# Kernel tuning notes

Measured on AMD Instinct MI355X. Metric: run time of the kernel, lower is better.

Reference implementation:

```python
import jax, jax.numpy as jnp
import numpy as np

T, B, N, D, O = 128, 8, 512, 256, 1


def _xavier(key, shape):
    # matches nn.init.xavier_normal_ (gain=1): std = sqrt(2/(fan_in+fan_out))
    std = np.sqrt(2.0 / (shape[0] + shape[1])).astype(np.float32)
    return jax.random.normal(key, shape, jnp.float32) * std


def setup_inputs() -> dict:
    key = jax.random.key(0)
    ks = jax.random.split(key, 7)
    return {
        "x": jax.random.normal(ks[0], (T, B, D), jnp.float32),
        "w_mult": _xavier(ks[1], (N, D)),
        "b_mult": _xavier(ks[2], (N, 1))[:, 0],   # stored (N,1) in torch; used as bias vector
        "w_add": _xavier(ks[3], (N, N)),
        "b_add": _xavier(ks[4], (N, 1))[:, 0],
        "w_final": _xavier(ks[5], (O, N)),
        "b_final": _xavier(ks[6], (O, 1))[:, 0],
        "lmbda_mult": jnp.float32(1.0),
        "lmbda_add": jnp.float32(1.0),
        "eta_mult": jnp.float32(-0.5),
        "eta_add": jnp.float32(-0.5),
        "Store": 0,
        "Batch": 0,
    }


def reference(x, w_mult, b_mult, w_add, b_add, w_final, b_final,
              lmbda_mult, lmbda_add, eta_mult, eta_add, Store, Batch):
    # Store=False / Batch=False branch of HebbFF, vmapped over B sequences
    # and scanned over T timesteps. Fast-weight state: A_mult [B,N,D], A_add [B,N,N].
    Bt = x.shape[1]
    Nh, Dd = w_mult.shape
    lam_m = jax.nn.sigmoid(lmbda_mult)
    lam_a = jax.nn.sigmoid(lmbda_add)

    def step(carry, x_t):
        A_m, A_a = carry                      # [B,N,D], [B,N,N]
        # h_mult = tanh((w_mult * A_mult) @ x + w_mult @ x + b_mult)
        h_m = jnp.tanh(jnp.einsum('bnd,bd->bn', w_mult * A_m, x_t)
                       + x_t @ w_mult.T + b_mult)          # [B,N]
        A_m = lam_m * A_m + eta_mult * jnp.einsum('bn,bd->bnd', h_m, x_t)
        # h_add = sigmoid((w_add + A_add) @ h_mult + b_add)
        h_a = jax.nn.sigmoid(jnp.einsum('bnm,bm->bn', A_a, h_m)
                             + h_m @ w_add.T + b_add)      # [B,N]
        A_a = lam_a * A_a + eta_add * jnp.einsum('bn,bm->bnm', h_a, h_m)
        y_t = jax.nn.sigmoid(h_a @ w_final.T + b_final)    # [B,O]
        return (A_m, A_a), y_t

    A_m0 = jnp.zeros((Bt, Nh, Dd), x.dtype)
    A_a0 = jnp.zeros((Bt, Nh, Nh), x.dtype)
    _, ys = jax.lax.scan(step, (A_m0, A_a0), x)            # ys: [T,B,O]
    return ys
```

## Files before the change

### kernel.cpp

```cpp
#include <hip/hip_runtime.h>
#include <cstdint>


#define T_ 128
#define B_ 8
#define N_ 512
#define D_ 256
#define HP_OFF 0
#define Z0_OFF 524288
#define WS_OFF 1048576
#define WS_NEED ((size_t)(1048576 + 131072) * 4)
#define HOFF (T_ * B_ * N_)
#define CH 16
#define NC (T_ / CH)

typedef float v2f __attribute__((ext_vector_type(2)));

__device__ __forceinline__ v2f v2(float s) { v2f r; r.x = s; r.y = s; return r; }
__device__ __forceinline__ v2f mk2(float a, float b) { v2f r; r.x = a; r.y = b; return r; }

__device__ __forceinline__ void load_lds16(const float* g, float* l) {
  __builtin_amdgcn_global_load_lds(
      (const __attribute__((address_space(1))) uint32_t*)(const void*)g,
      (__attribute__((address_space(3))) uint32_t*)(void*)l, 16, 0, 0);
}

#define DPP1(v, ctrl)                                                          \
  v += __int_as_float(                                                         \
      __builtin_amdgcn_update_dpp(0, __float_as_int(v), ctrl, 0xf, 0xf, true))

__device__ __forceinline__ float dpp_red(float v) {
  DPP1(v, 0x111); DPP1(v, 0x112); DPP1(v, 0x114); DPP1(v, 0x118);
  DPP1(v, 0x142); DPP1(v, 0x143);
  return v;
}
__device__ __forceinline__ v2f dpp_red2(v2f v) {
  float a = v.x, b = v.y;
  DPP1(a, 0x111); DPP1(b, 0x111); DPP1(a, 0x112); DPP1(b, 0x112);
  DPP1(a, 0x114); DPP1(b, 0x114); DPP1(a, 0x118); DPP1(b, 0x118);
  DPP1(a, 0x142); DPP1(b, 0x142); DPP1(a, 0x143); DPP1(b, 0x143);
  v.x = a; v.y = b;
  return v;
}
__device__ __forceinline__ float dpp_red1_32(float v) {
  DPP1(v, 0x111); DPP1(v, 0x112); DPP1(v, 0x114); DPP1(v, 0x118);
  DPP1(v, 0x142);
  return v;
}
__device__ __forceinline__ v2f dpp_red2_32(v2f v) {
  float a = v.x, b = v.y;
  DPP1(a, 0x111); DPP1(b, 0x111); DPP1(a, 0x112); DPP1(b, 0x112);
  DPP1(a, 0x114); DPP1(b, 0x114); DPP1(a, 0x118); DPP1(b, 0x118);
  DPP1(a, 0x142); DPP1(b, 0x142);
  v.x = a; v.y = b;
  return v;
}
__device__ __forceinline__ float dpp_wave_sum(float v) {
  v = dpp_red(v);
  return __int_as_float(__builtin_amdgcn_readlane(__float_as_int(v), 63));
}
__device__ __forceinline__ float sigmoid_f(float z) {
  return __builtin_amdgcn_rcpf(1.f + __expf(-z));
}
__device__ __forceinline__ float tanh_f(float z) {
  return 1.f - 2.f * __builtin_amdgcn_rcpf(1.f + __expf(2.f * z));
}

__global__ void __launch_bounds__(512, 1)
np_part1(const float* __restrict__ x, const float* __restrict__ w_mult,
         const float* __restrict__ b_mult, const float* __restrict__ p_lm,
         const float* __restrict__ p_em, float* __restrict__ ws) {
  const int g = blockIdx.x & 7, sub = blockIdx.x >> 3;
  const int wave = threadIdx.x >> 6, lane = threadIdx.x & 63;
  const int l31 = lane & 31, half = lane >> 5;
  const int n0 = (sub * 8 + wave) * 2;
  const int n = n0 + half;

  __shared__ float xs[T_][D_];
#pragma unroll
  for (int i = 0; i < 16; ++i) {
    const int r = wave * 16 + i;
    load_lds16(&x[(r * B_ + g) * D_ + 4 * lane], &xs[r][0]);
  }

  const float lam = sigmoid_f(p_lm[0]);
  const float eta = p_em[0];
  const v2f lam2 = v2(lam), klam2 = v2(1.f - lam);

  v2f wm[4], Bm[4];
#pragma unroll
  for (int c = 0; c < 4; ++c) {
    wm[c] = *(const v2f*)&w_mult[n * D_ + 64 * c + 2 * l31];
    Bm[c] = v2(1.f);
  }
  const float bm = b_mult[n];
  __syncthreads();

  float* hp = ws + HP_OFF;
  v2f xv[4][4];
#define LDX(slot, t)                                                           \
  {                                                                            \
    _Pragma("unroll") for (int c = 0; c < 4; ++c)                              \
        xv[slot][c] = *(const v2f*)&xs[t][64 * c + 2 * l31];                   \
  }
  LDX(0, 0) LDX(1, 1) LDX(2, 2)

  float ph = 0.f;
  for (int t4 = 0; t4 < T_; t4 += 4) {
#pragma unroll
    for (int j = 0; j < 4; ++j) {
      const int t = t4 + j;
      if (t + 3 < T_) LDX((j + 3) & 3, t + 3)
      v2f wx = wm[0] * xv[j][0];
      v2f a = wx * Bm[0];
#pragma unroll
      for (int c = 1; c < 4; ++c) {
        wx = wm[c] * xv[j][c];
        a = __builtin_elementwise_fma(wx, Bm[c], a);
      }
      float s = dpp_red1_32(a.x + a.y);
      const float zr0 =
          __int_as_float(__builtin_amdgcn_readlane(__float_as_int(s), 31));
      const float zr1 =
          __int_as_float(__builtin_amdgcn_readlane(__float_as_int(s), 63));
      const float zz = (half ? zr1 : zr0) + bm;
      const float hm = tanh_f(zz);
      const v2f c2 = v2(eta * hm);
#pragma unroll
      for (int c = 0; c < 4; ++c) {
        v2f inner = __builtin_elementwise_fma(c2, xv[j][c], klam2);
        Bm[c] = __builtin_elementwise_fma(lam2, Bm[c], inner);
      }
      if (j & 1) {
        if (l31 == 31)
          *(v2f*)(hp + (size_t)((t >> 1) * B_ + g) * (N_ * 2) + n * 2) =
              mk2(ph, hm);
      } else {
        ph = hm;
      }
    }
  }
#undef LDX
}

__global__ void __launch_bounds__(512)
np_mid(const float* __restrict__ w_add, const float* __restrict__ p_la,
       const float* __restrict__ p_ea, float* __restrict__ ws) {
  __shared__ float hl[8192];
  const int wave = threadIdx.x >> 6, lane = threadIdx.x & 63;
  const float* hp = ws + HP_OFF;
  float* z0 = ws + Z0_OFF;
  float* Wsc = ws + WS_OFF;

  if (blockIdx.x < 64) {
    const int b = blockIdx.x & 7, qq = blockIdx.x >> 3;
    const int hlf = wave >> 2, w4 = wave & 3;
    const int q = hlf ? (15 - qq) : qq;
    float* hb = hl + hlf * 4096;
    const float lam = sigmoid_f(p_la[0]);
    const float eta = p_ea[0];
#pragma unroll
    for (int i = 0; i < 4; ++i)
      load_lds16(&hp[((q * 4 + w4) * 8 + b) * 1024 + i * 256 + 4 * lane],
                 &hb[w4 * 1024 + i * 256]);
    __syncthreads();
    v2f hv[4][8];
#pragma unroll
    for (int i = 0; i < 4; ++i)
#pragma unroll
      for (int j = 0; j < 8; ++j)
        hv[i][j] = ((const v2f*)hb)[i * 512 + lane + 64 * j];

    const float l2lam = __log2f(lam);
    const int tlim = q * 8 + 7;
    float wv[8], wvn[8];
    auto loadg = [&](float* dst, int tp) {
      const float* hrow = hp + ((tp >> 1) * 8 + b) * 1024 + (tp & 1);
#pragma unroll
      for (int j = 0; j < 8; ++j) dst[j] = hrow[2 * (lane + 64 * j)];
    };
    if (w4 < tlim) loadg(wv, w4);
    for (int tp = w4; tp < tlim; tp += 4) {
      if (tp + 4 < tlim) loadg(wvn, tp + 4);
#pragma unroll
      for (int i = 0; i < 4; ++i) {
        v2f a = hv[i][0] * v2(wv[0]);
#pragma unroll
        for (int j = 1; j < 8; ++j)
          a = __builtin_elementwise_fma(hv[i][j], v2(wv[j]), a);
        a = dpp_red2(a);
        if (lane == 63) {
          const int te = q * 8 + 2 * i;
          if (tp < te)
            Wsc[(b * T_ + te) * T_ + tp] =
                eta * exp2f(l2lam * (float)(te - 1 - tp)) * a.x;
          if (tp < te + 1)
            Wsc[(b * T_ + te + 1) * T_ + tp] =
                eta * exp2f(l2lam * (float)(te - tp)) * a.y;
        }
      }
#pragma unroll
      for (int j = 0; j < 8; ++j) wv[j] = wvn[j];
    }
  } else {
    const int bx = blockIdx.x - 64;
    const int pr = bx >> 1;
    const int nh = bx & 1;
    if (wave < 4)
      load_lds16(&hp[pr * 1024 + wave * 256 + 4 * lane], &hl[wave * 256]);
    __syncthreads();

    const int l31 = lane & 31, half = lane >> 5;
    float4 hfa[4], hfb[4];
#pragma unroll
    for (int jj = 0; jj < 4; ++jj) {
      hfa[jj] = *(const float4*)&hl[256 * jj + 8 * l31];
      hfb[jj] = *(const float4*)&hl[256 * jj + 8 * l31 + 4];
    }
    const int rowe = 16 * (pr >> 3) + (pr & 7);
    const int nbase = nh * 256 + wave * 32;
    float4 wc[4], wn[4];
    auto loadw = [&](float4* dst, int n_) {
      const float* wr = w_add + (size_t)n_ * N_ + 4 * l31;
#pragma unroll
      for (int jj = 0; jj < 4; ++jj) dst[jj] = *(const float4*)&wr[128 * jj];
    };
    loadw(wc, nbase + half);
    for (int i = 0; i < 16; ++i) {
      if (i + 1 < 16) loadw(wn, nbase + 2 * (i + 1) + half);
      v2f a = v2(0.f);
#pragma unroll
      for (int jj = 0; jj < 4; ++jj) {
        a = __builtin_elementwise_fma(mk2(hfa[jj].x, hfa[jj].y), v2(wc[jj].x), a);
        a = __builtin_elementwise_fma(mk2(hfa[jj].z, hfa[jj].w), v2(wc[jj].y), a);
        a = __builtin_elementwise_fma(mk2(hfb[jj].x, hfb[jj].y), v2(wc[jj].z), a);
        a = __builtin_elementwise_fma(mk2(hfb[jj].z, hfb[jj].w), v2(wc[jj].w), a);
      }
      a = dpp_red2_32(a);
      if (l31 == 31) {
        const int n_ = nbase + 2 * i + half;
        z0[rowe * N_ + n_] = a.x;
        z0[(rowe + 8) * N_ + n_] = a.y;
      }
#pragma unroll
      for (int jj = 0; jj < 4; ++jj) wc[jj] = wn[jj];
    }
  }
}

__global__ void __launch_bounds__(512, 1)
np_scan(const float* __restrict__ b_add, float* __restrict__ ws) {
  __shared__ float Wl[T_][T_];
  __shared__ float ul[T_][64];
  __shared__ float zx[16][64];
  const int b = blockIdx.x >> 3, nc = blockIdx.x & 7;
  const int wave = threadIdx.x >> 6, lane = threadIdx.x & 63;
  float* z0 = ws + Z0_OFF;
  const float* Wb = ws + WS_OFF + b * T_ * T_;

#pragma unroll
  for (int i = 0; i < 8; ++i) {
    const int r2 = wave * 16 + i * 2;
    load_lds16(&Wb[r2 * T_ + 4 * lane], &Wl[r2][0]);
  }

  const int ta = 2 * wave, tb2 = 2 * wave + 1;
  const int ncol = nc * 64 + lane;
  const float ban = b_add[ncol];

  float za = z0[(ta * B_ + b) * N_ + ncol] + ban;
  float zb = z0[(tb2 * B_ + b) * N_ + ncol] + ban;
  __syncthreads();

  for (int j = 0; j < 8; ++j) {
    const int t0 = j * 16;
    float zna = 0.f, znb = 0.f;
    if (j < 7) {
      zna = z0[((t0 + 16 + ta) * B_ + b) * N_ + ncol] + ban;
      znb = z0[((t0 + 16 + tb2) * B_ + b) * N_ + ncol] + ban;
    }
    float ha0 = 0.f, ha1 = 0.f, hb0 = 0.f, hb1 = 0.f;
#pragma unroll 2
    for (int s4 = 0; s4 < t0; s4 += 4) {
      const float4 wa = *(const float4*)&Wl[t0 + ta][s4];
      const float4 wb = *(const float4*)&Wl[t0 + tb2][s4];
      const float u0 = ul[s4 + 0][lane], u1 = ul[s4 + 1][lane];
      const float u2 = ul[s4 + 2][lane], u3 = ul[s4 + 3][lane];
      ha0 = __builtin_fmaf(wa.x, u0, ha0);
      ha1 = __builtin_fmaf(wa.y, u1, ha1);
      ha0 = __builtin_fmaf(wa.z, u2, ha0);
      ha1 = __builtin_fmaf(wa.w, u3, ha1);
      hb0 = __builtin_fmaf(wb.x, u0, hb0);
      hb1 = __builtin_fmaf(wb.y, u1, hb1);
      hb0 = __builtin_fmaf(wb.z, u2, hb0);
      hb1 = __builtin_fmaf(wb.w, u3, hb1);
    }
    zx[ta][lane] = za + (ha0 + ha1);
    zx[tb2][lane] = zb + (hb0 + hb1);
    __syncthreads();
    if (wave == 0) {
      float z[16], uv[16];
#pragma unroll
      for (int i = 0; i < 16; ++i) z[i] = zx[i][lane];
#pragma unroll
      for (int i = 0; i < 16; ++i) {
        const float u = sigmoid_f(z[i]);
        uv[i] = u;
        z0[((t0 + i) * B_ + b) * N_ + ncol] = u;
#pragma unroll
        for (int tt = i + 1; tt < 16; ++tt)
          z[tt] = __builtin_fmaf(u, Wl[t0 + tt][t0 + i], z[tt]);
      }
#pragma unroll
      for (int i = 0; i < 16; ++i) ul[t0 + i][lane] = uv[i];
    }
    __syncthreads();
    za = zna;
    zb = znb;
  }
}

__global__ void __launch_bounds__(512)
np_final(const float* __restrict__ ws, const float* __restrict__ w_final,
         const float* __restrict__ b_final, float* __restrict__ out) {
  const int wave = threadIdx.x >> 6, lane = threadIdx.x & 63;
  const int tb = blockIdx.x * 8 + wave;
  const float* u = ws + Z0_OFF + tb * N_ + lane * 8;
  const float4 a = *(const float4*)u, c = *(const float4*)(u + 4);
  const float4 wa = *(const float4*)&w_final[lane * 8];
  const float4 wc = *(const float4*)&w_final[lane * 8 + 4];
  float d = a.x * wa.x + a.y * wa.y + a.z * wa.z + a.w * wa.w +
            c.x * wc.x + c.y * wc.y + c.z * wc.z + c.w * wc.w;
  d = dpp_wave_sum(d);
  if (lane == 0) out[tb] = sigmoid_f(d + b_final[0]);
}


__global__ void __launch_bounds__(512, 2)
fb_part1(const float* __restrict__ x, const float* __restrict__ w_mult,
         const float* __restrict__ b_mult, const float* __restrict__ p_lm,
         const float* __restrict__ p_em, float* __restrict__ ws) {
  const int g = blockIdx.x & 7, sub = blockIdx.x >> 3;
  const int wave = threadIdx.x >> 6, lane = threadIdx.x & 63;
  const int n0 = (sub * 8 + wave) * 2;
  __shared__ float xs[2][CH][D_];
  const float lam = sigmoid_f(p_lm[0]);
  const float eta = p_em[0];
  const v2f lam2 = v2(lam), klam2 = v2(1.f - lam);
  v2f wm[2][2], Bm[2][2];
  float bm[2];
#pragma unroll
  for (int r = 0; r < 2; ++r) {
    bm[r] = b_mult[n0 + r];
#pragma unroll
    for (int c = 0; c < 2; ++c) {
      wm[r][c] = *(const v2f*)&w_mult[(n0 + r) * D_ + c * 128 + 2 * lane];
      Bm[r][c] = v2(1.f);
    }
  }
  auto issue_stage = [&](int c) {
#pragma unroll
    for (int k = 0; k < 2; ++k) {
      const int row = k * 8 + wave;
      load_lds16(&x[((c * CH + row) * B_ + g) * D_ + 4 * lane],
                 &xs[c & 1][row][0]);
    }
  };
  issue_stage(0);
  __syncthreads();
  v2f xv[2][2];
  auto ldx = [&](int buf, int cb, int tl) {
    xv[buf][0] = *(const v2f*)&xs[cb][tl][2 * lane];
    xv[buf][1] = *(const v2f*)&xs[cb][tl][128 + 2 * lane];
  };
  for (int c = 0; c < NC; ++c) {
    if (c + 1 < NC) issue_stage(c + 1);
    const int cb = c & 1;
    ldx(0, cb, 0);
#pragma unroll
    for (int tl = 0; tl < CH; ++tl) {
      const int buf = tl & 1;
      if (tl + 1 < CH) ldx(buf ^ 1, cb, tl + 1);
      float hmv[2];
#pragma unroll
      for (int r = 0; r < 2; ++r) {
        v2f a = wm[r][0] * xv[buf][0] * Bm[r][0];
        a = __builtin_elementwise_fma(wm[r][1] * xv[buf][1], Bm[r][1], a);
        const float z = dpp_wave_sum(a.x + a.y) + bm[r];
        const float hm = tanh_f(z);
        hmv[r] = hm;
        const v2f c2 = v2(eta * hm);
#pragma unroll
        for (int cc = 0; cc < 2; ++cc) {
          v2f inner = __builtin_elementwise_fma(c2, xv[buf][cc], klam2);
          Bm[r][cc] = __builtin_elementwise_fma(lam2, Bm[r][cc], inner);
        }
      }
      if (lane == 0) {
        v2f hv2;
        hv2.x = hmv[0];
        hv2.y = hmv[1];
        *(v2f*)(ws + ((c * CH + tl) * B_ + g) * N_ + n0) = hv2;
      }
    }
    __syncthreads();
  }
}

__global__ void __launch_bounds__(512, 2)
fb_part2(const float* __restrict__ w_add, const float* __restrict__ b_add,
         const float* __restrict__ w_final, const float* __restrict__ p_la,
         const float* __restrict__ p_ea, float* __restrict__ ws) {
  const int g = blockIdx.x & 7, sub = blockIdx.x >> 3;
  const int wave = threadIdx.x >> 6, lane = threadIdx.x & 63;
  const int n0 = (sub * 8 + wave) * 2;
  __shared__ float hs[2][CH][N_];
  const float lam = sigmoid_f(p_la[0]);
  const float eta = p_ea[0];
  const v2f lam2 = v2(lam);
  const float klam = 1.f - lam;
  v2f Sa[2][4], wb[2][4];
  float ba[2], wf[2];
#pragma unroll
  for (int r = 0; r < 2; ++r) {
    ba[r] = b_add[n0 + r];
    wf[r] = w_final[n0 + r];
#pragma unroll
    for (int c = 0; c < 4; ++c) {
      const v2f wa = *(const v2f*)&w_add[(n0 + r) * N_ + c * 128 + 2 * lane];
      Sa[r][c] = wa;
      wb[r][c] = wa * klam;
    }
  }
  const float* hsrc = ws;
  float* part = ws + HOFF;
  auto issue_stage = [&](int c) {
#pragma unroll
    for (int k = 0; k < 2; ++k) {
      const int row = k * 8 + wave;
#pragma unroll
      for (int jj = 0; jj < 2; ++jj)
        load_lds16(&hsrc[((c * CH + row) * B_ + g) * N_ + jj * 256 + 4 * lane],
                   &hs[c & 1][row][jj * 256]);
    }
  };
  issue_stage(0);
  __syncthreads();
  v2f hv[2][4];
  auto ldh = [&](int buf, int cb, int tl) {
#pragma unroll
    for (int cc = 0; cc < 4; ++cc)
      hv[buf][cc] = *(const v2f*)&hs[cb][tl][cc * 128 + 2 * lane];
  };
  for (int c = 0; c < NC; ++c) {
    if (c + 1 < NC) issue_stage(c + 1);
    const int cb = c & 1;
    ldh(0, cb, 0);
#pragma unroll
    for (int tl = 0; tl < CH; ++tl) {
      const int buf = tl & 1;
      if (tl + 1 < CH) ldh(buf ^ 1, cb, tl + 1);
      float py = 0.f;
#pragma unroll
      for (int r = 0; r < 2; ++r) {
        v2f a0 = Sa[r][0] * hv[buf][0];
        v2f a1 = Sa[r][1] * hv[buf][1];
        a0 = __builtin_elementwise_fma(Sa[r][2], hv[buf][2], a0);
        a1 = __builtin_elementwise_fma(Sa[r][3], hv[buf][3], a1);
        const v2f a = a0 + a1;
        const float z = dpp_wave_sum(a.x + a.y) + ba[r];
        const float ha = sigmoid_f(z);
        const v2f c2 = v2(eta * ha);
#pragma unroll
        for (int cc = 0; cc < 4; ++cc) {
          v2f inner = __builtin_elementwise_fma(c2, hv[buf][cc], wb[r][cc]);
          Sa[r][cc] = __builtin_elementwise_fma(lam2, Sa[r][cc], inner);
        }
        py = __builtin_fmaf(wf[r], ha, py);
      }
      if (lane == 0)
        part[((c * CH + tl) * B_ + g) * 256 + sub * 8 + wave] = py;
    }
    __syncthreads();
  }
}

__global__ void __launch_bounds__(512)
fb_final(const float* __restrict__ ws, const float* __restrict__ b_final,
         float* __restrict__ out) {
  const int wave = threadIdx.x >> 6, lane = threadIdx.x & 63;
  const int tb = blockIdx.x * 8 + wave;
  const float4 v = *(const float4*)(ws + HOFF + tb * 256 + lane * 4);
  const float s = dpp_wave_sum((v.x + v.y) + (v.z + v.w));
  if (lane == 0) out[tb] = sigmoid_f(s + b_final[0]);
}


extern "C" void kernel_launch(void* const* d_in, const int* in_sizes, int n_in,
                              void* d_out, int out_size, void* d_ws,
                              size_t ws_size, hipStream_t stream) {
  const float* x       = (const float*)d_in[0];
  const float* w_mult  = (const float*)d_in[1];
  const float* b_mult  = (const float*)d_in[2];
  const float* w_add   = (const float*)d_in[3];
  const float* b_add   = (const float*)d_in[4];
  const float* w_final = (const float*)d_in[5];
  const float* b_final = (const float*)d_in[6];
  const float* p_lm    = (const float*)d_in[7];
  const float* p_la    = (const float*)d_in[8];
  const float* p_em    = (const float*)d_in[9];
  const float* p_ea    = (const float*)d_in[10];
  float* out = (float*)d_out;
  float* ws  = (float*)d_ws;

  if (ws_size >= WS_NEED) {
    hipLaunchKernelGGL(np_part1, dim3(256), dim3(512), 0, stream,
                       x, w_mult, b_mult, p_lm, p_em, ws);
    hipLaunchKernelGGL(np_mid, dim3(1088), dim3(512), 0, stream,
                       w_add, p_la, p_ea, ws);
    hipLaunchKernelGGL(np_scan, dim3(64), dim3(512), 0, stream, b_add, ws);
    hipLaunchKernelGGL(np_final, dim3(128), dim3(512), 0, stream,
                       ws, w_final, b_final, out);
  } else {
    hipLaunchKernelGGL(fb_part1, dim3(256), dim3(512), 0, stream,
                       x, w_mult, b_mult, p_lm, p_em, ws);
    hipLaunchKernelGGL(fb_part2, dim3(256), dim3(512), 0, stream,
                       w_add, b_add, w_final, p_la, p_ea, ws);
    hipLaunchKernelGGL(fb_final, dim3(128), dim3(512), 0, stream,
                       ws, b_final, out);
  }
}
```

Before: 88.46 us.

## Restructure np_mid z0 GEMM to keep w_add tiles in registers and stream h

The z0 = h·w_addᵀ part of np_mid now gives each block a group of 64 output columns and 16 h row pairs. Each lane holds 4 w_add rows in registers and streams h rows from global memory with double buffering, instead of loading one h pair into LDS and re-streaming w_add rows per block. This cuts the grid from 1088 to 320 blocks and makes stores float4-wide, reducing redundant w_add traffic. Launch bounds now request 2 blocks per CU, which may limit registers given the larger register-resident tile.

```diff
diff --git a/kernel.cpp b/kernel.cpp
--- a/kernel.cpp
+++ b/kernel.cpp
@@ -143,7 +143,7 @@
 #undef LDX
 }
 
-__global__ void __launch_bounds__(512)
+__global__ void __launch_bounds__(512, 2)
 np_mid(const float* __restrict__ w_add, const float* __restrict__ p_la,
        const float* __restrict__ p_ea, float* __restrict__ ws) {
   __shared__ float hl[8192];
@@ -204,46 +204,63 @@
     }
   } else {
     const int bx = blockIdx.x - 64;
-    const int pr = bx >> 1;
-    const int nh = bx & 1;
-    if (wave < 4)
-      load_lds16(&hp[pr * 1024 + wave * 256 + 4 * lane], &hl[wave * 256]);
-    __syncthreads();
-
+    const int ng = bx >> 5;
+    const int pg = bx & 31;
     const int l31 = lane & 31, half = lane >> 5;
-    float4 hfa[4], hfb[4];
-#pragma unroll
-    for (int jj = 0; jj < 4; ++jj) {
-      hfa[jj] = *(const float4*)&hl[256 * jj + 8 * l31];
-      hfb[jj] = *(const float4*)&hl[256 * jj + 8 * l31 + 4];
-    }
-    const int rowe = 16 * (pr >> 3) + (pr & 7);
-    const int nbase = nh * 256 + wave * 32;
-    float4 wc[4], wn[4];
-    auto loadw = [&](float4* dst, int n_) {
-      const float* wr = w_add + (size_t)n_ * N_ + 4 * l31;
-#pragma unroll
-      for (int jj = 0; jj < 4; ++jj) dst[jj] = *(const float4*)&wr[128 * jj];
+    const int nb = ng * 64 + wave * 8 + half * 4;
+
+    float4 wreg[4][4];
+#pragma unroll
+    for (int i = 0; i < 4; ++i) {
+      const float* wr = w_add + (size_t)(nb + i) * N_ + 4 * l31;
+#pragma unroll
+      for (int jj = 0; jj < 4; ++jj)
+        wreg[i][jj] = *(const float4*)&wr[128 * jj];
+    }
+
+    const float* hbase = hp + (size_t)pg * 16 * 1024 + 8 * l31;
+    float4 hA[8], hB[8];
+    auto loadh = [&](float4* dst, int it) {
+      const float* hr = hbase + it * 1024;
+#pragma unroll
+      for (int jj = 0; jj < 4; ++jj) {
+        dst[2 * jj] = *(const float4*)&hr[256 * jj];
+        dst[2 * jj + 1] = *(const float4*)&hr[256 * jj + 4];
+      }
     };
-    loadw(wc, nbase + half);
-    for (int i = 0; i < 16; ++i) {
-      if (i + 1 < 16) loadw(wn, nbase + 2 * (i + 1) + half);
-      v2f a = v2(0.f);
-#pragma unroll
-      for (int jj = 0; jj < 4; ++jj) {
-        a = __builtin_elementwise_fma(mk2(hfa[jj].x, hfa[jj].y), v2(wc[jj].x), a);
-        a = __builtin_elementwise_fma(mk2(hfa[jj].z, hfa[jj].w), v2(wc[jj].y), a);
-        a = __builtin_elementwise_fma(mk2(hfb[jj].x, hfb[jj].y), v2(wc[jj].z), a);
-        a = __builtin_elementwise_fma(mk2(hfb[jj].z, hfb[jj].w), v2(wc[jj].w), a);
-      }
-      a = dpp_red2_32(a);
+    auto compute = [&](const float4* hc, int it) {
+      const int pr = pg * 16 + it;
+      const int rowe = 16 * (pr >> 3) + (pr & 7);
+      float ev[4], od[4];
+#pragma unroll
+      for (int i = 0; i < 4; ++i) {
+        v2f a = v2(0.f);
+#pragma unroll
+        for (int jj = 0; jj < 4; ++jj) {
+          const float4 w4 = wreg[i][jj];
+          const float4 h0 = hc[2 * jj], h1 = hc[2 * jj + 1];
+          a = __builtin_elementwise_fma(mk2(h0.x, h0.y), v2(w4.x), a);
+          a = __builtin_elementwise_fma(mk2(h0.z, h0.w), v2(w4.y), a);
+          a = __builtin_elementwise_fma(mk2(h1.x, h1.y), v2(w4.z), a);
+          a = __builtin_elementwise_fma(mk2(h1.z, h1.w), v2(w4.w), a);
+        }
+        a = dpp_red2_32(a);
+        ev[i] = a.x;
+        od[i] = a.y;
+      }
       if (l31 == 31) {
-        const int n_ = nbase + 2 * i + half;
-        z0[rowe * N_ + n_] = a.x;
-        z0[(rowe + 8) * N_ + n_] = a.y;
-      }
-#pragma unroll
-      for (int jj = 0; jj < 4; ++jj) wc[jj] = wn[jj];
+        *(float4*)&z0[rowe * N_ + nb] = make_float4(ev[0], ev[1], ev[2], ev[3]);
+        *(float4*)&z0[(rowe + 8) * N_ + nb] =
+            make_float4(od[0], od[1], od[2], od[3]);
+      }
+    };
+
+    loadh(hA, 0);
+    for (int it = 0; it < 16; it += 2) {
+      loadh(hB, it + 1);
+      compute(hA, it);
+      if (it + 2 < 16) loadh(hA, it + 2);
+      compute(hB, it + 1);
     }
   }
 }
@@ -516,7 +533,7 @@
   if (ws_size >= WS_NEED) {
     hipLaunchKernelGGL(np_part1, dim3(256), dim3(512), 0, stream,
                        x, w_mult, b_mult, p_lm, p_em, ws);
-    hipLaunchKernelGGL(np_mid, dim3(1088), dim3(512), 0, stream,
+    hipLaunchKernelGGL(np_mid, dim3(320), dim3(512), 0, stream,
                        w_add, p_la, p_ea, ws);
     hipLaunchKernelGGL(np_scan, dim3(64), dim3(512), 0, stream, b_add, ws);
     hipLaunchKernelGGL(np_final, dim3(128), dim3(512), 0, stream,
```

Result: faster. 85.49 us (-3.4%).

## Split mid kernel into register-tiled base GEMM and separate Gram kernel

Applied to the files above, without the earlier changes.

The combined np_mid kernel is split into two launches. np_base now keeps four w_add rows in registers per half-wave and streams h pairs from global memory with double-buffered loads, reusing each h load across four output rows. The old version reloaded w_add rows per output and held one h pair per block. np_gram keeps the same Gram-matrix computation but uses explicit scalar double-buffering. This adds a kernel launch and gives up the overlap of the two heterogeneous workloads within one grid.

```diff
diff --git a/kernel.cpp b/kernel.cpp
--- a/kernel.cpp
+++ b/kernel.cpp
@@ -66,6 +66,28 @@
   return 1.f - 2.f * __builtin_amdgcn_rcpf(1.f + __expf(2.f * z));
 }
 
+__device__ __forceinline__ v2f dot8p(float4 w0, float4 w1, float4 w2, float4 w3,
+                                     float4 h0, float4 h1, float4 h2, float4 h3,
+                                     float4 h4, float4 h5, float4 h6, float4 h7) {
+  v2f a = mk2(h0.x, h0.y) * v2(w0.x);
+  a = __builtin_elementwise_fma(mk2(h0.z, h0.w), v2(w0.y), a);
+  a = __builtin_elementwise_fma(mk2(h1.x, h1.y), v2(w0.z), a);
+  a = __builtin_elementwise_fma(mk2(h1.z, h1.w), v2(w0.w), a);
+  a = __builtin_elementwise_fma(mk2(h2.x, h2.y), v2(w1.x), a);
+  a = __builtin_elementwise_fma(mk2(h2.z, h2.w), v2(w1.y), a);
+  a = __builtin_elementwise_fma(mk2(h3.x, h3.y), v2(w1.z), a);
+  a = __builtin_elementwise_fma(mk2(h3.z, h3.w), v2(w1.w), a);
+  a = __builtin_elementwise_fma(mk2(h4.x, h4.y), v2(w2.x), a);
+  a = __builtin_elementwise_fma(mk2(h4.z, h4.w), v2(w2.y), a);
+  a = __builtin_elementwise_fma(mk2(h5.x, h5.y), v2(w2.z), a);
+  a = __builtin_elementwise_fma(mk2(h5.z, h5.w), v2(w2.w), a);
+  a = __builtin_elementwise_fma(mk2(h6.x, h6.y), v2(w3.x), a);
+  a = __builtin_elementwise_fma(mk2(h6.z, h6.w), v2(w3.y), a);
+  a = __builtin_elementwise_fma(mk2(h7.x, h7.y), v2(w3.z), a);
+  a = __builtin_elementwise_fma(mk2(h7.z, h7.w), v2(w3.w), a);
+  return a;
+}
+
 __global__ void __launch_bounds__(512, 1)
 np_part1(const float* __restrict__ x, const float* __restrict__ w_mult,
          const float* __restrict__ b_mult, const float* __restrict__ p_lm,
@@ -143,109 +165,152 @@
 #undef LDX
 }
 
-__global__ void __launch_bounds__(512)
-np_mid(const float* __restrict__ w_add, const float* __restrict__ p_la,
-       const float* __restrict__ p_ea, float* __restrict__ ws) {
-  __shared__ float hl[8192];
-  const int wave = threadIdx.x >> 6, lane = threadIdx.x & 63;
+__global__ void __launch_bounds__(512, 1)
+np_base(const float* __restrict__ w_add, float* __restrict__ ws) {
+  const int ng = blockIdx.x >> 5, pg = blockIdx.x & 31;
+  const int wave = threadIdx.x >> 6, lane = threadIdx.x & 63;
+  const int l31 = lane & 31, half = lane >> 5;
+  const int nb = ng * 64 + wave * 8 + half * 4;
   const float* hp = ws + HP_OFF;
   float* z0 = ws + Z0_OFF;
+
+  float4 wreg[4][4];
+#pragma unroll
+  for (int i = 0; i < 4; ++i) {
+    const float* wr = w_add + (size_t)(nb + i) * N_ + 4 * l31;
+#pragma unroll
+    for (int jj = 0; jj < 4; ++jj)
+      wreg[i][jj] = *(const float4*)&wr[128 * jj];
+  }
+
+  const float* hbase = hp + (size_t)pg * 16 * 1024 + 8 * l31;
+
+#define LDH(h0, h1, h2, h3, h4, h5, h6, h7, it)                                \
+  do {                                                                         \
+    const float* hr_ = hbase + (size_t)(it) * 1024;                            \
+    h0 = *(const float4*)&hr_[0];                                              \
+    h1 = *(const float4*)&hr_[4];                                              \
+    h2 = *(const float4*)&hr_[256];                                            \
+    h3 = *(const float4*)&hr_[260];                                            \
+    h4 = *(const float4*)&hr_[512];                                            \
+    h5 = *(const float4*)&hr_[516];                                            \
+    h6 = *(const float4*)&hr_[768];                                            \
+    h7 = *(const float4*)&hr_[772];                                            \
+  } while (0)
+
+#define CMPB(h0, h1, h2, h3, h4, h5, h6, h7, it)                               \
+  do {                                                                         \
+    const int pr_ = pg * 16 + (it);                                            \
+    const int rowe_ = 16 * (pr_ >> 3) + (pr_ & 7);                             \
+    v2f a0_ = dot8p(wreg[0][0], wreg[0][1], wreg[0][2], wreg[0][3],            \
+                    h0, h1, h2, h3, h4, h5, h6, h7);                           \
+    v2f a1_ = dot8p(wreg[1][0], wreg[1][1], wreg[1][2], wreg[1][3],            \
+                    h0, h1, h2, h3, h4, h5, h6, h7);                           \
+    v2f a2_ = dot8p(wreg[2][0], wreg[2][1], wreg[2][2], wreg[2][3],            \
+                    h0, h1, h2, h3, h4, h5, h6, h7);                           \
+    v2f a3_ = dot8p(wreg[3][0], wreg[3][1], wreg[3][2], wreg[3][3],            \
+                    h0, h1, h2, h3, h4, h5, h6, h7);                           \
+    a0_ = dpp_red2_32(a0_);                                                    \
+    a1_ = dpp_red2_32(a1_);                                                    \
+    a2_ = dpp_red2_32(a2_);                                                    \
+    a3_ = dpp_red2_32(a3_);                                                    \
+    if (l31 == 31) {                                                           \
+      *(float4*)&z0[rowe_ * N_ + nb] =                                         \
+          make_float4(a0_.x, a1_.x, a2_.x, a3_.x);                             \
+      *(float4*)&z0[(rowe_ + 8) * N_ + nb] =                                   \
+          make_float4(a0_.y, a1_.y, a2_.y, a3_.y);                             \
+    }                                                                          \
+  } while (0)
+
+  float4 A0, A1, A2, A3, A4, A5, A6, A7;
+  float4 B0, B1, B2, B3, B4, B5, B6, B7;
+  LDH(A0, A1, A2, A3, A4, A5, A6, A7, 0);
+  for (int it = 0; it < 16; it += 2) {
+    LDH(B0, B1, B2, B3, B4, B5, B6, B7, it + 1);
+    CMPB(A0, A1, A2, A3, A4, A5, A6, A7, it);
+    if (it + 2 < 16) LDH(A0, A1, A2, A3, A4, A5, A6, A7, it + 2);
+    CMPB(B0, B1, B2, B3, B4, B5, B6, B7, it + 1);
+  }
+#undef LDH
+#undef CMPB
+}
+
+__global__ void __launch_bounds__(512, 1)
+np_gram(const float* __restrict__ p_la, const float* __restrict__ p_ea,
+        float* __restrict__ ws) {
+  __shared__ float hl[8192];
+  const int wave = threadIdx.x >> 6, lane = threadIdx.x & 63;
+  const float* hp = ws + HP_OFF;
   float* Wsc = ws + WS_OFF;
-
-  if (blockIdx.x < 64) {
-    const int b = blockIdx.x & 7, qq = blockIdx.x >> 3;
-    const int hlf = wave >> 2, w4 = wave & 3;
-    const int q = hlf ? (15 - qq) : qq;
-    float* hb = hl + hlf * 4096;
-    const float lam = sigmoid_f(p_la[0]);
-    const float eta = p_ea[0];
-#pragma unroll
-    for (int i = 0; i < 4; ++i)
-      load_lds16(&hp[((q * 4 + w4) * 8 + b) * 1024 + i * 256 + 4 * lane],
-                 &hb[w4 * 1024 + i * 256]);
-    __syncthreads();
-    v2f hv[4][8];
-#pragma unroll
-    for (int i = 0; i < 4; ++i)
-#pragma unroll
-      for (int j = 0; j < 8; ++j)
-        hv[i][j] = ((const v2f*)hb)[i * 512 + lane + 64 * j];
-
-    const float l2lam = __log2f(lam);
-    const int tlim = q * 8 + 7;
-    float wv[8], wvn[8];
-    auto loadg = [&](float* dst, int tp) {
-      const float* hrow = hp + ((tp >> 1) * 8 + b) * 1024 + (tp & 1);
-#pragma unroll
-      for (int j = 0; j < 8; ++j) dst[j] = hrow[2 * (lane + 64 * j)];
-    };
-    if (w4 < tlim) loadg(wv, w4);
-    for (int tp = w4; tp < tlim; tp += 4) {
-      if (tp + 4 < tlim) loadg(wvn, tp + 4);
-#pragma unroll
-      for (int i = 0; i < 4; ++i) {
-        v2f a = hv[i][0] * v2(wv[0]);
-#pragma unroll
-        for (int j = 1; j < 8; ++j)
-          a = __builtin_elementwise_fma(hv[i][j], v2(wv[j]), a);
-        a = dpp_red2(a);
-        if (lane == 63) {
-          const int te = q * 8 + 2 * i;
-          if (tp < te)
-            Wsc[(b * T_ + te) * T_ + tp] =
-                eta * exp2f(l2lam * (float)(te - 1 - tp)) * a.x;
-          if (tp < te + 1)
-            Wsc[(b * T_ + te + 1) * T_ + tp] =
-                eta * exp2f(l2lam * (float)(te - tp)) * a.y;
-        }
-      }
-#pragma unroll
-      for (int j = 0; j < 8; ++j) wv[j] = wvn[j];
-    }
-  } else {
-    const int bx = blockIdx.x - 64;
-    const int pr = bx >> 1;
-    const int nh = bx & 1;
-    if (wave < 4)
-      load_lds16(&hp[pr * 1024 + wave * 256 + 4 * lane], &hl[wave * 256]);
-    __syncthreads();
-
-    const int l31 = lane & 31, half = lane >> 5;
-    float4 hfa[4], hfb[4];
-#pragma unroll
-    for (int jj = 0; jj < 4; ++jj) {
-      hfa[jj] = *(const float4*)&hl[256 * jj + 8 * l31];
-      hfb[jj] = *(const float4*)&hl[256 * jj + 8 * l31 + 4];
-    }
-    const int rowe = 16 * (pr >> 3) + (pr & 7);
-    const int nbase = nh * 256 + wave * 32;
-    float4 wc[4], wn[4];
-    auto loadw = [&](float4* dst, int n_) {
-      const float* wr = w_add + (size_t)n_ * N_ + 4 * l31;
-#pragma unroll
-      for (int jj = 0; jj < 4; ++jj) dst[jj] = *(const float4*)&wr[128 * jj];
-    };
-    loadw(wc, nbase + half);
-    for (int i = 0; i < 16; ++i) {
-      if (i + 1 < 16) loadw(wn, nbase + 2 * (i + 1) + half);
-      v2f a = v2(0.f);
-#pragma unroll
-      for (int jj = 0; jj < 4; ++jj) {
-        a = __builtin_elementwise_fma(mk2(hfa[jj].x, hfa[jj].y), v2(wc[jj].x), a);
-        a = __builtin_elementwise_fma(mk2(hfa[jj].z, hfa[jj].w), v2(wc[jj].y), a);
-        a = __builtin_elementwise_fma(mk2(hfb[jj].x, hfb[jj].y), v2(wc[jj].z), a);
-        a = __builtin_elementwise_fma(mk2(hfb[jj].z, hfb[jj].w), v2(wc[jj].w), a);
-      }
-      a = dpp_red2_32(a);
-      if (l31 == 31) {
-        const int n_ = nbase + 2 * i + half;
-        z0[rowe * N_ + n_] = a.x;
-        z0[(rowe + 8) * N_ + n_] = a.y;
-      }
-#pragma unroll
-      for (int jj = 0; jj < 4; ++jj) wc[jj] = wn[jj];
-    }
-  }
+  const int b = blockIdx.x & 7, qq = blockIdx.x >> 3;
+  const int hlf = wave >> 2, w4 = wave & 3;
+  const int q = hlf ? (15 - qq) : qq;
+  float* hb = hl + hlf * 4096;
+  const float lam = sigmoid_f(p_la[0]);
+  const float eta = p_ea[0];
+#pragma unroll
+  for (int i = 0; i < 4; ++i)
+    load_lds16(&hp[((q * 4 + w4) * 8 + b) * 1024 + i * 256 + 4 * lane],
+               &hb[w4 * 1024 + i * 256]);
+  __syncthreads();
+  v2f hv[4][8];
+#pragma unroll
+  for (int i = 0; i < 4; ++i)
+#pragma unroll
+    for (int j = 0; j < 8; ++j)
+      hv[i][j] = ((const v2f*)hb)[i * 512 + lane + 64 * j];
+
+  const float l2lam = __log2f(lam);
+  const int tlim = q * 8 + 7;
+
+#define LDG(p0, p1, p2, p3, p4, p5, p6, p7, tp)                                \
+  do {                                                                         \
+    const float* hr_ = hp + (((tp) >> 1) * 8 + b) * 1024 + ((tp) & 1);         \
+    p0 = hr_[2 * lane];                                                        \
+    p1 = hr_[2 * lane + 128];                                                  \
+    p2 = hr_[2 * lane + 256];                                                  \
+    p3 = hr_[2 * lane + 384];                                                  \
+    p4 = hr_[2 * lane + 512];                                                  \
+    p5 = hr_[2 * lane + 640];                                                  \
+    p6 = hr_[2 * lane + 768];                                                  \
+    p7 = hr_[2 * lane + 896];                                                  \
+  } while (0)
+
+#define CMPG(p0, p1, p2, p3, p4, p5, p6, p7, tp)                               \
+  do {                                                                         \
+    _Pragma("unroll") for (int i_ = 0; i_ < 4; ++i_) {                         \
+      v2f a_ = hv[i_][0] * v2(p0);                                             \
+      a_ = __builtin_elementwise_fma(hv[i_][1], v2(p1), a_);                   \
+      a_ = __builtin_elementwise_fma(hv[i_][2], v2(p2), a_);                   \
+      a_ = __builtin_elementwise_fma(hv[i_][3], v2(p3), a_);                   \
+      a_ = __builtin_elementwise_fma(hv[i_][4], v2(p4), a_);                   \
+      a_ = __builtin_elementwise_fma(hv[i_][5], v2(p5), a_);                   \
+      a_ = __builtin_elementwise_fma(hv[i_][6], v2(p6), a_);                   \
+      a_ = __builtin_elementwise_fma(hv[i_][7], v2(p7), a_);                   \
+      a_ = dpp_red2(a_);                                                       \
+      if (lane == 63) {                                                        \
+        const int te_ = q * 8 + 2 * i_;                                        \
+        if ((tp) < te_)                                                        \
+          Wsc[(b * T_ + te_) * T_ + (tp)] =                                    \
+              eta * exp2f(l2lam * (float)(te_ - 1 - (tp))) * a_.x;             \
+        if ((tp) < te_ + 1)                                                    \
+          Wsc[(b * T_ + te_ + 1) * T_ + (tp)] =                                \
+              eta * exp2f(l2lam * (float)(te_ - (tp))) * a_.y;                 \
+      }                                                                        \
+    }                                                                          \
+  } while (0)
+
+  float ra0, ra1, ra2, ra3, ra4, ra5, ra6, ra7;
+  float rb0, rb1, rb2, rb3, rb4, rb5, rb6, rb7;
+  if (w4 < tlim) LDG(ra0, ra1, ra2, ra3, ra4, ra5, ra6, ra7, w4);
+  for (int tp = w4; tp < tlim; tp += 4) {
+    if (tp + 4 < tlim) LDG(rb0, rb1, rb2, rb3, rb4, rb5, rb6, rb7, tp + 4);
+    CMPG(ra0, ra1, ra2, ra3, ra4, ra5, ra6, ra7, tp);
+    ra0 = rb0; ra1 = rb1; ra2 = rb2; ra3 = rb3;
+    ra4 = rb4; ra5 = rb5; ra6 = rb6; ra7 = rb7;
+  }
+#undef LDG
+#undef CMPG
 }
 
 __global__ void __launch_bounds__(512, 1)
@@ -516,8 +581,9 @@
   if (ws_size >= WS_NEED) {
     hipLaunchKernelGGL(np_part1, dim3(256), dim3(512), 0, stream,
                        x, w_mult, b_mult, p_lm, p_em, ws);
-    hipLaunchKernelGGL(np_mid, dim3(1088), dim3(512), 0, stream,
-                       w_add, p_la, p_ea, ws);
+    hipLaunchKernelGGL(np_base, dim3(256), dim3(512), 0, stream, w_add, ws);
+    hipLaunchKernelGGL(np_gram, dim3(64), dim3(512), 0, stream,
+                       p_la, p_ea, ws);
     hipLaunchKernelGGL(np_scan, dim3(64), dim3(512), 0, stream, b_add, ws);
     hipLaunchKernelGGL(np_final, dim3(128), dim3(512), 0, stream,
                        ws, w_final, b_final, out);
```

New measurement: 100.1 us. 13.1% more time.
